# Optimization experiments

Hardware: AMD Instinct MI355X
Metric: run time of the kernel (lower is better)

The kernel has to match this reference:

```python
import jax, jax.numpy as jnp
import numpy as np

LOG2E = 1.4426950408889634  # 1/ln(2): convert natural-log gates to log2 space (kernel uses exp2)
BT = 64  # chunk size


def setup_inputs() -> dict:
    key = jax.random.key(0)
    ks = jax.random.split(key, 5)
    B, H, T, K, V = 4, 8, 4096, 128, 128
    return {
        "q": jax.random.normal(ks[0], (B, H, T, K), dtype=jnp.float32),
        "k": jax.random.normal(ks[1], (B, H, T, K), dtype=jnp.float32),
        "v": jax.random.normal(ks[2], (B, H, T, V), dtype=jnp.float32),
        "i_gate": jax.random.normal(ks[3], (B, H, T), dtype=jnp.float32),
        "f_gate": jax.random.normal(ks[4], (B, H, T), dtype=jnp.float32),
    }


def reference(q, k, v, i_gate, f_gate):
    B, H, T, K = q.shape
    V = v.shape[-1]
    NT = T // BT
    scale = K ** -0.5

    # gate preprocessing: log-sigmoid forget gate, both gates moved to log2 space
    vecF = jax.nn.log_sigmoid(f_gate) * LOG2E  # [B,H,T]
    vecI = i_gate * LOG2E                      # [B,H,T]

    f_c = vecF.reshape(B, H, NT, BT)
    i_c = vecI.reshape(B, H, NT, BT)
    qc = q.reshape(B, H, NT, BT, K)
    kc = k.reshape(B, H, NT, BT, K)
    vc = v.reshape(B, H, NT, BT, V)

    vecB = jnp.cumsum(f_c, axis=-1)            # inclusive cumsum of f within chunk [B,H,NT,BT]
    scaG = vecB[..., -1]                       # total decay per chunk [B,H,NT]
    vecA = i_c + (scaG[..., None] - vecB)      # i_j + sum of f after j within chunk

    # ---- inter-chunk recurrence over matrix state C, normalizer n, max m ----
    kx = jnp.moveaxis(kc, 2, 0)  # [NT,B,H,BT,K]
    vx = jnp.moveaxis(vc, 2, 0)
    ax = jnp.moveaxis(vecA, 2, 0)  # [NT,B,H,BT]
    gx = jnp.moveaxis(scaG, 2, 0)  # [NT,B,H]

    C0 = jnp.zeros((B, H, K, V), dtype=q.dtype)
    n0 = jnp.zeros((B, H, K), dtype=q.dtype)
    m0 = jnp.zeros((B, H), dtype=q.dtype)

    def step(carry, inp):
        C, n, m = carry
        kk, vv, a, g = inp
        m_next = jnp.maximum(g + m, jnp.max(a, axis=-1))      # running stabilizer max
        dec = jnp.exp2(g + m - m_next)                        # [B,H]
        kbar = kk * jnp.exp2(a - m_next[..., None])[..., None]
        C_next = C * dec[..., None, None] + jnp.einsum('bhtk,bhtv->bhkv', kbar, vv)
        n_next = n * dec[..., None] + kbar.sum(axis=-2)
        return (C_next, n_next, m_next), (C, n, m)

    _, (Cp, np_, mp) = jax.lax.scan(step, (C0, n0, m0), (kx, vx, ax, gx))
    Cp = jnp.moveaxis(Cp, 0, 2)   # state entering each chunk [B,H,NT,K,V]
    np_ = jnp.moveaxis(np_, 0, 2)  # [B,H,NT,K]
    mp = jnp.moveaxis(mp, 0, 2)   # [B,H,NT]

    # ---- intra-chunk parallel part ----
    idx = jnp.arange(BT)
    causal = idx[:, None] >= idx[None, :]  # query i attends key j<=i
    # logD[i,j] = B_i - B_j + I_j for j<=i
    logD = vecB[..., :, None] - vecB[..., None, :] + i_c[..., None, :]
    logD = jnp.where(causal, logD, -jnp.inf)
    m_intra = logD.max(axis=-1)                                   # [B,H,NT,BT]
    m_comb = jnp.maximum(mp[..., None] + vecB, m_intra)           # total stabilizer per row
    D = jnp.exp2(logD - m_comb[..., None])                        # masked entries -> 0

    S = jnp.einsum('bhcik,bhcjk->bhcij', qc, kc) * scale * D
    qbar = qc * (scale * jnp.exp2(vecB + mp[..., None] - m_comb))[..., None]

    Hnum = jnp.einsum('bhcik,bhckv->bhciv', qbar, Cp) + jnp.einsum('bhcij,bhcjv->bhciv', S, vc)
    den = jnp.einsum('bhcik,bhck->bhci', qbar, np_) + S.sum(axis=-1)
    norm = jnp.maximum(jnp.abs(den), jnp.exp2(-m_comb))
    h = Hnum / norm[..., None]
    return h.reshape(B, H, T, V)
```

## Files before the change

kernel.cpp:

```cpp
#include <hip/hip_runtime.h>
#include <hip/hip_bf16.h>
#include <math.h>


#define LOG2E 1.4426950408889634f
constexpr int Bsz = 4, Hsz = 8, Tsz = 4096, Ksz = 128, Vsz = 128;
constexpr int BT = 64, NT = 64, BH = Bsz * Hsz;
constexpr float SCALE = 0.08838834764831845f;

typedef __attribute__((ext_vector_type(8))) short short8v;
typedef __attribute__((ext_vector_type(4))) float f32x4;
typedef __attribute__((ext_vector_type(4))) unsigned short u16x4;
typedef __attribute__((ext_vector_type(8))) unsigned short u16x8;

__device__ inline float bf2f(unsigned short u) {
    union { unsigned int i; float f; } c; c.i = ((unsigned int)u) << 16; return c.f;
}
__device__ inline unsigned short f2bf(float f) {
    union { float f; unsigned int i; } c; c.f = f;
    unsigned int x = c.i;
    x += 0x7fffu + ((x >> 16) & 1u);
    return (unsigned short)(x >> 16);
}

__global__ __launch_bounds__(64) void k_gates(
    const float* __restrict__ ig, const float* __restrict__ fg,
    float* __restrict__ vecB, float* __restrict__ vecI, float* __restrict__ vecA,
    float* __restrict__ mintra, float* __restrict__ scaG, float* __restrict__ scaA)
{
    int c = blockIdx.x, bh = blockIdx.y, lane = threadIdx.x;
    int t = bh * Tsz + c * BT + lane;
    float f = fg[t];
    float ls = fminf(f, 0.f) - log1pf(expf(-fabsf(f)));
    float vF = ls * LOG2E;
    float vI = ig[t] * LOG2E;
    float b = vF;
    #pragma unroll
    for (int off = 1; off < 64; off <<= 1) {
        float o = __shfl_up(b, off, 64);
        if (lane >= off) b += o;
    }
    float g = __shfl(b, 63, 64);
    float mi = vI - b;
    #pragma unroll
    for (int off = 1; off < 64; off <<= 1) {
        float o = __shfl_up(mi, off, 64);
        if (lane >= off) mi = fmaxf(mi, o);
    }
    float a = vI + g - b;
    vecB[t] = b; vecI[t] = vI; vecA[t] = a; mintra[t] = b + mi;
    float am = a;
    #pragma unroll
    for (int off = 32; off; off >>= 1) am = fmaxf(am, __shfl_xor(am, off, 64));
    if (lane == 0) { scaG[bh * NT + c] = g; scaA[bh * NT + c] = am; }
}

__global__ __launch_bounds__(64) void k_mscan(
    const float* __restrict__ scaG, const float* __restrict__ scaA,
    float* __restrict__ mp, float* __restrict__ dec)
{
    int bh = blockIdx.x, lane = threadIdx.x;
    float g0 = scaG[bh * NT + lane];
    float a = g0, b = scaA[bh * NT + lane];
    #pragma unroll
    for (int off = 1; off < 64; off <<= 1) {
        float ap = __shfl_up(a, off, 64);
        float bp = __shfl_up(b, off, 64);
        if (lane >= off) { b = fmaxf(bp + a, b); a = ap + a; }
    }
    float m_incl = fmaxf(a, b);
    float m_prev = __shfl_up(m_incl, 1, 64);
    if (lane == 0) { m_prev = 0.f; mp[bh * (NT + 1)] = 0.f; }
    mp[bh * (NT + 1) + lane + 1] = m_incl;
    dec[bh * NT + lane] = exp2f(g0 + m_prev - m_incl);
}

__global__ __launch_bounds__(256, 3) void k_state(
    const float* __restrict__ kg, const float* __restrict__ vg,
    const float* __restrict__ vecA, const float* __restrict__ mp,
    unsigned short* __restrict__ UT, float* __restrict__ nU)
{
    int c = blockIdx.x, bh = blockIdx.y, tid = threadIdx.x;
    int lane = tid & 63, wid = tid >> 6;
    int lrow = lane & 15, kgrp = lane >> 4;

    __shared__ __align__(16) unsigned short kThi[128][72];
    __shared__ __align__(16) unsigned short vTs[128][72];
    __shared__ float nUp[128][17];

    size_t hb = (size_t)bh * Tsz + (size_t)c * BT;
    float mpn = mp[bh * (NT + 1) + c + 1];

    int cb = tid & 15, jr = tid >> 4;
    float s4[4];
    #pragma unroll
    for (int x = 0; x < 4; ++x) s4[x] = exp2f(vecA[hb + jr * 4 + x] - mpn);
    #pragma unroll
    for (int p = 0; p < 2; ++p) {
        int c0 = p * 64 + cb * 4;
        float ka[4][4], va[4][4];
        #pragma unroll
        for (int x = 0; x < 4; ++x) {
            float4 kr = *(const float4*)(kg + (hb + jr * 4 + x) * Ksz + c0);
            float4 vr = *(const float4*)(vg + (hb + jr * 4 + x) * Vsz + c0);
            ka[x][0] = kr.x; ka[x][1] = kr.y; ka[x][2] = kr.z; ka[x][3] = kr.w;
            va[x][0] = vr.x; va[x][1] = vr.y; va[x][2] = vr.z; va[x][3] = vr.w;
        }
        #pragma unroll
        for (int y = 0; y < 4; ++y) {
            u16x4 h, w;
            float psum = 0.f;
            #pragma unroll
            for (int x = 0; x < 4; ++x) {
                float f = ka[x][y] * s4[x];
                h[x] = f2bf(f);
                psum += f;
                w[x] = f2bf(va[x][y]);
            }
            *(u16x4*)&kThi[c0 + y][jr * 4] = h;
            *(u16x4*)&vTs[c0 + y][jr * 4] = w;
            nUp[c0 + y][jr] = psum;
        }
    }
    __syncthreads();

    f32x4 acc[2][8];
    #pragma unroll
    for (int kt = 0; kt < 2; ++kt)
        #pragma unroll
        for (int vt = 0; vt < 8; ++vt) acc[kt][vt] = (f32x4){0.f, 0.f, 0.f, 0.f};
    #pragma unroll
    for (int ks = 0; ks < 2; ++ks) {
        #pragma unroll
        for (int kt = 0; kt < 2; ++kt) {
            short8v af = *(const short8v*)&kThi[(wid * 2 + kt) * 16 + lrow][ks * 32 + kgrp * 8];
            #pragma unroll
            for (int vt = 0; vt < 8; ++vt) {
                short8v bv = *(const short8v*)&vTs[vt * 16 + lrow][ks * 32 + kgrp * 8];
                acc[kt][vt] = __builtin_amdgcn_mfma_f32_16x16x32_bf16(af, bv, acc[kt][vt], 0, 0, 0);
            }
        }
    }
    unsigned short* Ub = UT + (size_t)(bh * NT + c) * (Ksz * Vsz);
    #pragma unroll
    for (int kt = 0; kt < 2; ++kt)
        #pragma unroll
        for (int vt = 0; vt < 8; ++vt) {
            int vc = vt * 16 + lrow;
            int k0 = (wid * 2 + kt) * 16 + kgrp * 4;
            u16x4 w;
            #pragma unroll
            for (int r = 0; r < 4; ++r) w[r] = f2bf(acc[kt][vt][r]);
            *(u16x4*)(Ub + (size_t)vc * Ksz + k0) = w;
        }
    if (tid < Ksz) {
        float ssum = 0.f;
        #pragma unroll
        for (int j = 0; j < 16; ++j) ssum += nUp[tid][j];
        nU[(size_t)(bh * NT + c) * Ksz + tid] = ssum;
    }
}

__global__ __launch_bounds__(128) void k_scan(
    unsigned short* __restrict__ UT, const float* __restrict__ dec,
    const float* __restrict__ nU, float* __restrict__ np)
{
    int s = blockIdx.x, bh = blockIdx.y, tid = threadIdx.x;
    __shared__ float decs[NT];
    if (tid < NT) decs[tid] = dec[bh * NT + tid];
    __syncthreads();
    if (s == 32) {
        float n = 0.f;
        size_t base = (size_t)bh * NT * Ksz + tid;
        #pragma unroll 4
        for (int c2 = 0; c2 < NT; ++c2) {
            float u = nU[base + (size_t)c2 * Ksz];
            np[base + (size_t)c2 * Ksz] = n;
            n = n * decs[c2] + u;
        }
        return;
    }
    int vc = s * 4 + (tid >> 5), k0 = (tid & 31) * 4;
    size_t base = (size_t)bh * NT * (Ksz * Vsz) + (size_t)vc * Ksz + k0;
    float C0 = 0.f, C1 = 0.f, C2 = 0.f, C3 = 0.f;
    #pragma unroll 4
    for (int c2 = 0; c2 < NT; ++c2) {
        size_t idx = base + (size_t)c2 * (Ksz * Vsz);
        u16x4 u = *(const u16x4*)(UT + idx);
        u16x4 w;
        w.x = f2bf(C0); w.y = f2bf(C1); w.z = f2bf(C2); w.w = f2bf(C3);
        *(u16x4*)(UT + idx) = w;
        float d = decs[c2];
        C0 = C0 * d + bf2f(u.x); C1 = C1 * d + bf2f(u.y);
        C2 = C2 * d + bf2f(u.z); C3 = C3 * d + bf2f(u.w);
    }
}

__global__ __launch_bounds__(256, 4) void k_intra(
    const float* __restrict__ qg, const float* __restrict__ kgl, const float* __restrict__ vg,
    const float* __restrict__ vecB, const float* __restrict__ vecI,
    const float* __restrict__ mintra, const float* __restrict__ mp,
    const float* __restrict__ np, const unsigned short* __restrict__ CpT,
    float* __restrict__ out)
{
    int c = blockIdx.x, bh = blockIdx.y, tid = threadIdx.x;
    int lane = tid & 63, wid = tid >> 6;
    int lrow = lane & 15, kgrp = lane >> 4;

    __shared__ __align__(16) unsigned short R[17408];
    __shared__ float rowf[BT], colf[BT], sfqs[BT], emcs[BT], denb[BT], npv[Ksz];

    auto khi = (unsigned short(*)[136])R;
    auto klo = (unsigned short(*)[136])(R + 64 * 136);
    auto Sb  = (unsigned short(*)[72])R;
    unsigned short* vTf = R + 64 * 72;
    auto cps = (unsigned short(*)[136])R;

    size_t hb = (size_t)bh * Tsz + (size_t)c * BT;
    float mpc = mp[bh * (NT + 1) + c];
    if (tid < BT) {
        float b = vecB[hb + tid];
        float mc = fmaxf(mpc + b, mintra[hb + tid]);
        rowf[tid] = SCALE * exp2f(b - mc);
        colf[tid] = exp2f(vecI[hb + tid] - b);
        sfqs[tid] = SCALE * exp2f(b + mpc - mc);
        emcs[tid] = exp2f(-mc);
    }
    if (tid < Ksz) npv[tid] = np[((size_t)bh * NT + c) * Ksz + tid];

    const float4* k4 = (const float4*)(kgl + hb * Ksz);
    for (int e = tid; e < BT * Ksz / 4; e += 256) {
        int i = e >> 5, c4 = (e & 31) * 4;
        float4 kv = k4[e];
        u16x4 h, l;
        h.x = f2bf(kv.x); l.x = f2bf(kv.x - bf2f(h.x));
        h.y = f2bf(kv.y); l.y = f2bf(kv.y - bf2f(h.y));
        h.z = f2bf(kv.z); l.z = f2bf(kv.z - bf2f(h.z));
        h.w = f2bf(kv.w); l.w = f2bf(kv.w - bf2f(h.w));
        *(u16x4*)&khi[i][c4] = h; *(u16x4*)&klo[i][c4] = l;
    }
    const float* qrow = qg + (hb + wid * 16 + lrow) * Ksz;
    float qf[4][8];
    #pragma unroll
    for (int ks = 0; ks < 4; ++ks) {
        float4 a = *(const float4*)(qrow + ks * 32 + kgrp * 8);
        float4 b = *(const float4*)(qrow + ks * 32 + kgrp * 8 + 4);
        qf[ks][0] = a.x; qf[ks][1] = a.y; qf[ks][2] = a.z; qf[ks][3] = a.w;
        qf[ks][4] = b.x; qf[ks][5] = b.y; qf[ks][6] = b.z; qf[ks][7] = b.w;
    }
    int vcb = tid & 15, jb = tid >> 4;
    float vpre[2][4][4];
    #pragma unroll
    for (int p = 0; p < 2; ++p)
        #pragma unroll
        for (int x = 0; x < 4; ++x) {
            float4 r4 = *(const float4*)(vg + (hb + jb * 4 + x) * Vsz + p * 64 + vcb * 4);
            vpre[p][x][0] = r4.x; vpre[p][x][1] = r4.y; vpre[p][x][2] = r4.z; vpre[p][x][3] = r4.w;
        }
    __syncthreads();

    float dot = 0.f;
    #pragma unroll
    for (int ks = 0; ks < 4; ++ks)
        #pragma unroll
        for (int x = 0; x < 8; ++x) dot += qf[ks][x] * npv[ks * 32 + kgrp * 8 + x];
    dot += __shfl_xor(dot, 16, 64);
    dot += __shfl_xor(dot, 32, 64);
    float qdot = sfqs[wid * 16 + lrow] * dot;

    short8v qh[4], ql[4];
    #pragma unroll
    for (int ks = 0; ks < 4; ++ks)
        #pragma unroll
        for (int x = 0; x < 8; ++x) {
            float f = qf[ks][x];
            unsigned short hh = f2bf(f);
            qh[ks][x] = (short)hh;
            ql[ks][x] = (short)f2bf(f - bf2f(hh));
        }

    f32x4 accS[4];
    #pragma unroll
    for (int jt = 0; jt < 4; ++jt) accS[jt] = (f32x4){0.f, 0.f, 0.f, 0.f};
    #pragma unroll
    for (int ks = 0; ks < 4; ++ks) {
        #pragma unroll
        for (int jt = 0; jt < 4; ++jt) {
            if (jt <= wid) {
                short8v bh_ = *(const short8v*)&khi[jt * 16 + lrow][ks * 32 + kgrp * 8];
                short8v bl  = *(const short8v*)&klo[jt * 16 + lrow][ks * 32 + kgrp * 8];
                accS[jt] = __builtin_amdgcn_mfma_f32_16x16x32_bf16(qh[ks], bh_, accS[jt], 0, 0, 0);
                accS[jt] = __builtin_amdgcn_mfma_f32_16x16x32_bf16(ql[ks], bh_, accS[jt], 0, 0, 0);
                accS[jt] = __builtin_amdgcn_mfma_f32_16x16x32_bf16(qh[ks], bl,  accS[jt], 0, 0, 0);
            }
        }
    }

    float rsum[4] = {0.f, 0.f, 0.f, 0.f};
    unsigned short sreg[4][4];
    #pragma unroll
    for (int jt = 0; jt < 4; ++jt)
        #pragma unroll
        for (int r = 0; r < 4; ++r) {
            int i = wid * 16 + kgrp * 4 + r, j = jt * 16 + lrow;
            float val = (j <= i) ? accS[jt][r] * rowf[i] * colf[j] : 0.f;
            rsum[r] += val;
            sreg[jt][r] = f2bf(val);
        }
    #pragma unroll
    for (int r = 0; r < 4; ++r) {
        rsum[r] += __shfl_xor(rsum[r], 1, 64);
        rsum[r] += __shfl_xor(rsum[r], 2, 64);
        rsum[r] += __shfl_xor(rsum[r], 4, 64);
        rsum[r] += __shfl_xor(rsum[r], 8, 64);
    }
    float qd[4];
    #pragma unroll
    for (int r = 0; r < 4; ++r) qd[r] = __shfl(qdot, kgrp * 4 + r, 64);
    if (lrow == 0) {
        #pragma unroll
        for (int r = 0; r < 4; ++r) {
            int i = wid * 16 + kgrp * 4 + r;
            float den = qd[r] + rsum[r];
            denb[i] = 1.f / fmaxf(fabsf(den), emcs[i]);
        }
    }
    __syncthreads();

    const u16x8* Cg = (const u16x8*)(CpT + ((size_t)bh * NT + c) * (Ksz * Vsz));
    u16x8 cpre[8];
    #pragma unroll
    for (int p2 = 0; p2 < 8; ++p2) cpre[p2] = Cg[tid + p2 * 256];

    #pragma unroll
    for (int jt = 0; jt < 4; ++jt)
        #pragma unroll
        for (int r = 0; r < 4; ++r)
            Sb[wid * 16 + kgrp * 4 + r][jt * 16 + lrow] = sreg[jt][r];
    #pragma unroll
    for (int p = 0; p < 2; ++p)
        #pragma unroll
        for (int y = 0; y < 4; ++y) {
            int row = p * 64 + vcb * 4 + y;
            int swzb = (jb * 8) ^ ((row & 7) << 4);
            u16x4 w;
            #pragma unroll
            for (int x = 0; x < 4; ++x) w[x] = f2bf(vpre[p][x][y]);
            *(u16x4*)((char*)(vTf + row * 64) + swzb) = w;
        }
    __syncthreads();

    f32x4 accV[8];
    #pragma unroll
    for (int vt = 0; vt < 8; ++vt) accV[vt] = (f32x4){0.f, 0.f, 0.f, 0.f};
    #pragma unroll
    for (int ks = 0; ks < 2; ++ks) {
        short8v as_ = *(const short8v*)&Sb[wid * 16 + lrow][ks * 32 + kgrp * 8];
        #pragma unroll
        for (int vt = 0; vt < 8; ++vt) {
            int row = vt * 16 + lrow;
            int swzb = ((ks * 64 + kgrp * 16)) ^ ((row & 7) << 4);
            short8v bv = *(const short8v*)((const char*)(vTf + row * 64) + swzb);
            accV[vt] = __builtin_amdgcn_mfma_f32_16x16x32_bf16(as_, bv, accV[vt], 0, 0, 0);
        }
    }
    __syncthreads();

    #pragma unroll
    for (int p2 = 0; p2 < 8; ++p2) {
        int idx = tid + p2 * 256;
        *(u16x8*)&cps[idx >> 4][(idx & 15) * 8] = cpre[p2];
    }
    __syncthreads();

    f32x4 accC[8];
    #pragma unroll
    for (int vt = 0; vt < 8; ++vt) accC[vt] = (f32x4){0.f, 0.f, 0.f, 0.f};
    #pragma unroll
    for (int ks = 0; ks < 4; ++ks) {
        #pragma unroll
        for (int vt = 0; vt < 8; ++vt) {
            short8v bc = *(const short8v*)&cps[vt * 16 + lrow][ks * 32 + kgrp * 8];
            accC[vt] = __builtin_amdgcn_mfma_f32_16x16x32_bf16(qh[ks], bc, accC[vt], 0, 0, 0);
            accC[vt] = __builtin_amdgcn_mfma_f32_16x16x32_bf16(ql[ks], bc, accC[vt], 0, 0, 0);
        }
    }
    size_t gb = hb * Vsz;
    #pragma unroll
    for (int vt = 0; vt < 8; ++vt)
        #pragma unroll
        for (int r = 0; r < 4; ++r) {
            int i = wid * 16 + kgrp * 4 + r, vc = vt * 16 + lrow;
            out[gb + (size_t)i * Vsz + vc] = (sfqs[i] * accC[vt][r] + accV[vt][r]) * denb[i];
        }
}

extern "C" void kernel_launch(void* const* d_in, const int* in_sizes, int n_in,
                              void* d_out, int out_size, void* d_ws, size_t ws_size,
                              hipStream_t stream) {
    const float* q  = (const float*)d_in[0];
    const float* k  = (const float*)d_in[1];
    const float* v  = (const float*)d_in[2];
    const float* ig = (const float*)d_in[3];
    const float* fg = (const float*)d_in[4];
    float* out = (float*)d_out;

    float* ws = (float*)d_ws;
    float* vecB   = ws;
    float* vecI   = vecB + BH * Tsz;
    float* vecA   = vecI + BH * Tsz;
    float* mintra = vecA + BH * Tsz;
    float* scaG   = mintra + BH * Tsz;
    float* scaA   = scaG + BH * NT;
    float* dec    = scaA + BH * NT;
    float* mp     = dec + BH * NT;
    float* nU     = mp + BH * (NT + 1);
    float* np     = nU + BH * NT * Ksz;
    unsigned short* UT = (unsigned short*)(np + BH * NT * Ksz);

    k_gates<<<dim3(NT, BH), 64, 0, stream>>>(ig, fg, vecB, vecI, vecA, mintra, scaG, scaA);
    k_mscan<<<dim3(BH), 64, 0, stream>>>(scaG, scaA, mp, dec);
    k_state<<<dim3(NT, BH), 256, 0, stream>>>(k, v, vecA, mp, UT, nU);
    k_scan<<<dim3(33, BH), 128, 0, stream>>>(UT, dec, nU, np);
    k_intra<<<dim3(NT, BH), 256, 0, stream>>>(q, k, v, vecB, vecI, mintra, mp, np, UT, out);
}
```

Measured before the change: 125.9 us.

## Store chunk states in MFMA fragment order and reduce n-partials via shuffles

The per-chunk state matrices are now written in the MFMA accumulator fragment order, so each lane's 4 values form one contiguous 8-byte block and k_state writes are fully coalesced. The scan kernel and the intra kernel index this fragment layout directly; the intra kernel rebuilds its B operand from two 8-byte LDS reads in place of one 16-byte row read. The normalizer partial sums are reduced with cross-lane shuffles into a smaller LDS array, k_state occupancy is raised to 4 blocks, and bf16 conversion uses the HIP intrinsic. The split LDS reads may cost extra instructions or bank conflicts in k_intra.

After: 119.8 us. 4.8% less time.

```diff
diff --git a/kernel.cpp b/kernel.cpp
--- a/kernel.cpp
+++ b/kernel.cpp
@@ -17,10 +17,8 @@
     union { unsigned int i; float f; } c; c.i = ((unsigned int)u) << 16; return c.f;
 }
 __device__ inline unsigned short f2bf(float f) {
-    union { float f; unsigned int i; } c; c.f = f;
-    unsigned int x = c.i;
-    x += 0x7fffu + ((x >> 16) & 1u);
-    return (unsigned short)(x >> 16);
+    __hip_bfloat16 h = __float2bfloat16(f);
+    union { __hip_bfloat16 b; unsigned short u; } cv; cv.b = h; return cv.u;
 }
 
 __global__ __launch_bounds__(64) void k_gates(
@@ -75,7 +73,7 @@
     dec[bh * NT + lane] = exp2f(g0 + m_prev - m_incl);
 }
 
-__global__ __launch_bounds__(256, 3) void k_state(
+__global__ __launch_bounds__(256, 4) void k_state(
     const float* __restrict__ kg, const float* __restrict__ vg,
     const float* __restrict__ vecA, const float* __restrict__ mp,
     unsigned short* __restrict__ UT, float* __restrict__ nU)
@@ -86,7 +84,7 @@
 
     __shared__ __align__(16) unsigned short kThi[128][72];
     __shared__ __align__(16) unsigned short vTs[128][72];
-    __shared__ float nUp[128][17];
+    __shared__ float nUp[128][5];
 
     size_t hb = (size_t)bh * Tsz + (size_t)c * BT;
     float mpn = mp[bh * (NT + 1) + c + 1];
@@ -119,7 +117,9 @@
             }
             *(u16x4*)&kThi[c0 + y][jr * 4] = h;
             *(u16x4*)&vTs[c0 + y][jr * 4] = w;
-            nUp[c0 + y][jr] = psum;
+            psum += __shfl_xor(psum, 16, 64);
+            psum += __shfl_xor(psum, 32, 64);
+            if (kgrp == 0) nUp[c0 + y][wid] = psum;
         }
     }
     __syncthreads();
@@ -143,21 +143,19 @@
     }
     unsigned short* Ub = UT + (size_t)(bh * NT + c) * (Ksz * Vsz);
     #pragma unroll
-    for (int kt = 0; kt < 2; ++kt)
+    for (int kt = 0; kt < 2; ++kt) {
+        int ktile = wid * 2 + kt;
         #pragma unroll
         for (int vt = 0; vt < 8; ++vt) {
-            int vc = vt * 16 + lrow;
-            int k0 = (wid * 2 + kt) * 16 + kgrp * 4;
             u16x4 w;
             #pragma unroll
             for (int r = 0; r < 4; ++r) w[r] = f2bf(acc[kt][vt][r]);
-            *(u16x4*)(Ub + (size_t)vc * Ksz + k0) = w;
-        }
+            *(u16x4*)(Ub + ((size_t)(ktile * 8 + vt) * 64 + lane) * 4) = w;
+        }
+    }
     if (tid < Ksz) {
-        float ssum = 0.f;
-        #pragma unroll
-        for (int j = 0; j < 16; ++j) ssum += nUp[tid][j];
-        nU[(size_t)(bh * NT + c) * Ksz + tid] = ssum;
+        float s = nUp[tid][0] + nUp[tid][1] + nUp[tid][2] + nUp[tid][3];
+        nU[(size_t)(bh * NT + c) * Ksz + tid] = s;
     }
 }
 
@@ -180,8 +178,7 @@
         }
         return;
     }
-    int vc = s * 4 + (tid >> 5), k0 = (tid & 31) * 4;
-    size_t base = (size_t)bh * NT * (Ksz * Vsz) + (size_t)vc * Ksz + k0;
+    size_t base = (size_t)bh * NT * (Ksz * Vsz) + s * 512 + tid * 4;
     float C0 = 0.f, C1 = 0.f, C2 = 0.f, C3 = 0.f;
     #pragma unroll 4
     for (int c2 = 0; c2 < NT; ++c2) {
@@ -214,7 +211,7 @@
     auto klo = (unsigned short(*)[136])(R + 64 * 136);
     auto Sb  = (unsigned short(*)[72])R;
     unsigned short* vTf = R + 64 * 72;
-    auto cps = (unsigned short(*)[136])R;
+    unsigned short* cpsF = R;
 
     size_t hb = (size_t)bh * Tsz + (size_t)c * BT;
     float mpc = mp[bh * (NT + 1) + c];
@@ -369,7 +366,7 @@
     #pragma unroll
     for (int p2 = 0; p2 < 8; ++p2) {
         int idx = tid + p2 * 256;
-        *(u16x8*)&cps[idx >> 4][(idx & 15) * 8] = cpre[p2];
+        *(u16x8*)&cpsF[idx * 8] = cpre[p2];
     }
     __syncthreads();
 
@@ -378,9 +375,16 @@
     for (int vt = 0; vt < 8; ++vt) accC[vt] = (f32x4){0.f, 0.f, 0.f, 0.f};
     #pragma unroll
     for (int ks = 0; ks < 4; ++ks) {
+        int ktile = ks * 2 + (kgrp >> 1);
+        int lsrc = (kgrp & 1) * 32 + lrow;
         #pragma unroll
         for (int vt = 0; vt < 8; ++vt) {
-            short8v bc = *(const short8v*)&cps[vt * 16 + lrow][ks * 32 + kgrp * 8];
+            const unsigned short* pf = &cpsF[((ktile * 8 + vt) * 64 + lsrc) * 4];
+            u16x4 lo4 = *(const u16x4*)pf;
+            u16x4 hi4 = *(const u16x4*)(pf + 64);
+            short8v bc;
+            bc[0] = (short)lo4.x; bc[1] = (short)lo4.y; bc[2] = (short)lo4.z; bc[3] = (short)lo4.w;
+            bc[4] = (short)hi4.x; bc[5] = (short)hi4.y; bc[6] = (short)hi4.z; bc[7] = (short)hi4.w;
             accC[vt] = __builtin_amdgcn_mfma_f32_16x16x32_bf16(qh[ks], bc, accC[vt], 0, 0, 0);
             accC[vt] = __builtin_amdgcn_mfma_f32_16x16x32_bf16(ql[ks], bc, accC[vt], 0, 0, 0);
         }
```
